# Kernel optimization log

Hardware: AMD Instinct MI355X
Metric: run time of the kernel (lower is better)

Reference implementation:

```python
import jax, jax.numpy as jnp
import numpy as np
import math

COND_DIM = 64
HIDDEN = 128
NUM_SIN = 2
SQRT2 = 1.4142135623730951


def fused_leaky_relu(x, bias):
    # stylegan2 fused bias + leaky relu (slope 0.2) with sqrt(2) gain
    return jax.nn.leaky_relu(x + bias, negative_slope=0.2) * SQRT2


def equal_linear2(x, W, b, lr_mul=1.0, activation=False):
    scale = lr_mul / math.sqrt(W.shape[1])
    out = x @ (W * scale).T
    if activation:
        return fused_leaky_relu(out, b * lr_mul)
    return out + b * lr_mul


def coords_to_sinusoidals(x, num_sinusoidals=NUM_SIN, multiplier=2.0):
    # x: [P, 1] -> [P, 2*num_sinusoidals], freq_type='mult': freqs = multiplier**i
    freqs = multiplier ** jnp.arange(num_sinusoidals, dtype=x.dtype)  # [S]
    ang = x * freqs  # [P, S]
    return jnp.concatenate([jnp.sin(ang), jnp.cos(ang)], axis=-1)


def setup_inputs() -> dict:
    key = jax.random.key(0)
    ks = jax.random.split(key, 10)
    B, N = 64, 8192
    coord_in = 2 * NUM_SIN  # 4
    in1 = coord_in + COND_DIM  # 68
    in2 = HIDDEN + COND_DIM    # 192
    coords = jax.random.normal(ks[0], (B, N, 2), dtype=jnp.float32)
    c = jax.random.normal(ks[1], (B, N, COND_DIM), dtype=jnp.float32)
    # EqualLinear2 weights init uniform(-1,1)/lr_mul; last layer zero in torch,
    # use small random values here so gradients/outputs are non-trivial.
    Wx1 = jax.random.uniform(ks[2], (HIDDEN, in1), minval=-1.0, maxval=1.0)
    bx1 = jnp.zeros((HIDDEN,), jnp.float32)
    Wx2 = jax.random.uniform(ks[3], (2, in2), minval=-1.0, maxval=1.0) * 0.1
    bx2 = jnp.zeros((2,), jnp.float32)
    Wy1 = jax.random.uniform(ks[4], (HIDDEN, in1), minval=-1.0, maxval=1.0)
    by1 = jnp.zeros((HIDDEN,), jnp.float32)
    Wy2 = jax.random.uniform(ks[5], (2, in2), minval=-1.0, maxval=1.0) * 0.1
    by2 = jnp.zeros((2,), jnp.float32)
    return {"coords": coords, "c": c,
            "Wx1": Wx1, "bx1": bx1, "Wx2": Wx2, "bx2": bx2,
            "Wy1": Wy1, "by1": by1, "Wy2": Wy2, "by2": by2}


def reference(coords, c, Wx1, bx1, Wx2, bx2, Wy1, by1, Wy2, by2):
    initial_shape = coords.shape[:-1]
    coords2 = coords.reshape(-1, coords.shape[-1])  # [P, 2]
    cf = c.reshape(-1, c.shape[-1])                 # [P, cond]
    x = coords2[:, 0:1]
    y = coords2[:, 1:2]

    # x branch -> affine params for y
    h = coords_to_sinusoidals(x / 10.0)
    h = equal_linear2(jnp.concatenate([h, cf], -1), Wx1, bx1, activation=True)
    o = equal_linear2(jnp.concatenate([h, cf], -1), Wx2, bx2, activation=False)
    y_log_scale = jnp.clip(o[:, 0:1], -5.0, 5.0)
    y_bias = o[:, 1:2]
    y = y * jnp.exp(y_log_scale) + y_bias

    # y branch -> affine params for x
    h = coords_to_sinusoidals(y / 10.0)
    h = equal_linear2(jnp.concatenate([h, cf], -1), Wy1, by1, activation=True)
    o = equal_linear2(jnp.concatenate([h, cf], -1), Wy2, by2, activation=False)
    x_log_scale = jnp.clip(o[:, 0:1], -5.0, 5.0)
    x_bias = o[:, 1:2]
    x = x * jnp.exp(x_log_scale) + x_bias

    warped = jnp.concatenate([x, y], -1).reshape(*initial_shape, -1)
    log_jac = jnp.concatenate([x_log_scale + y_log_scale], -1)
    log_jac = (x_log_scale + y_log_scale).reshape(*initial_shape, -1)
    return warped, log_jac
```

## Files before the change

### kernel.cpp

```cpp
#include <hip/hip_runtime.h>

typedef unsigned short u16t;
typedef short short8 __attribute__((ext_vector_type(8)));
typedef float f32x4 __attribute__((ext_vector_type(4)));

__device__ __forceinline__ u16t f2bf_rne(float f) {
  unsigned u = __builtin_bit_cast(unsigned, f);
  u += 0x7FFFu + ((u >> 16) & 1u);
  return (u16t)(u >> 16);
}
__device__ __forceinline__ unsigned pk2(float a, float b) {
  unsigned ua = __builtin_bit_cast(unsigned, a) + 0x8000u;
  unsigned ub = __builtin_bit_cast(unsigned, b) + 0x8000u;
  return (ua >> 16) | (ub & 0xFFFF0000u);
}
union S8U { short8 s; unsigned w[4]; };
__device__ __forceinline__ short8 pack8f(float4 a, float4 b) {
  S8U u;
  u.w[0] = pk2(a.x, a.y); u.w[1] = pk2(a.z, a.w);
  u.w[2] = pk2(b.x, b.y); u.w[3] = pk2(b.z, b.w);
  return u.s;
}

#define WS_WB  0
#define WS_BS  32768
#define WS_FF  49152
#define WS_BC  65536

__global__ void prep_kernel(const float* __restrict__ Wx1, const float* __restrict__ bx1,
                            const float* __restrict__ Wx2,
                            const float* __restrict__ Wy1, const float* __restrict__ by1,
                            const float* __restrict__ Wy2,
                            char* __restrict__ ws)
{
  const int tid = threadIdx.x;
  const int p = tid >> 9, nt = (tid >> 6) & 7, lane = tid & 63;
  const int l15 = lane & 15, quad = lane >> 4;
  const float* W1 = p ? Wy1 : Wx1;
  const float* B1 = p ? by1 : bx1;
  const float* W2 = p ? Wy2 : Wx2;
  const int n = nt * 16 + l15;
  const float* rp = W1 + n * 68;
  short8 bb0, bb1, bs = (short8)0;
  #pragma unroll
  for (int j = 0; j < 8; ++j) {
    bb0[j] = (short)f2bf_rne(rp[4 + quad * 8 + j]);
    bb1[j] = (short)f2bf_rne(rp[36 + quad * 8 + j]);
  }
  if (quad == 0) {
    #pragma unroll
    for (int j = 0; j < 4; ++j) bs[j] = (short)f2bf_rne(rp[j]);
  }
  short8* wb = (short8*)(ws + WS_WB);
  wb[((p * 8 + nt) * 2 + 0) * 64 + lane] = bb0;
  wb[((p * 8 + nt) * 2 + 1) * 64 + lane] = bb1;
  ((short8*)(ws + WS_BS))[(p * 8 + nt) * 64 + lane] = bs;
  const float SQ2 = 1.41421356237309515f;
  float4 ff;
  ff.x = B1[n]; ff.y = W2[n] * SQ2; ff.z = W2[192 + n] * SQ2; ff.w = 0.f;
  ((float4*)(ws + WS_FF))[(p * 8 + nt) * 64 + lane] = ff;

  if (tid < 256) {
    const int p2 = tid >> 7, h = (tid >> 6) & 1, ln = tid & 63;
    const int l2 = ln & 15, q2 = ln >> 4;
    const float* W2b = p2 ? Wy2 : Wx2;
    short8 bc = (short8)0;
    if (l2 < 2) {
      #pragma unroll
      for (int j = 0; j < 8; ++j)
        bc[j] = (short)f2bf_rne(W2b[l2 * 192 + 128 + h * 32 + q2 * 8 + j]);
    }
    ((short8*)(ws + WS_BC))[(p2 * 2 + h) * 64 + ln] = bc;
  }
}

__global__ __launch_bounds__(256, 4)
void icb_main(const float* __restrict__ g_coords, const float* __restrict__ g_c,
              const float* __restrict__ g_bx2, const float* __restrict__ g_by2,
              const char* __restrict__ ws, float* __restrict__ g_out)
{
  const int tid  = threadIdx.x;
  const int lane = tid & 63, wave = tid >> 6;
  const int l15  = lane & 15, quad = lane >> 4;
  const int wbase = blockIdx.x * 128 + wave * 32;

  const short8* wb  = (const short8*)(ws + WS_WB);
  const short8* wbs = (const short8*)(ws + WS_BS);
  const float4* wf  = (const float4*)(ws + WS_FF);
  const short8* wbc = (const short8*)(ws + WS_BC);

  short8 aC0[2], aC1[2];
  float xold[2], yold[2];
  #pragma unroll
  for (int mt = 0; mt < 2; ++mt) {
    const int r = wbase + mt * 16 + l15;
    const float4* cr = (const float4*)(g_c + (size_t)r * 64);
    float4 a0 = cr[quad * 2],     a1 = cr[quad * 2 + 1];
    float4 a2 = cr[8 + quad * 2], a3 = cr[8 + quad * 2 + 1];
    aC0[mt] = pack8f(a0, a1);
    aC1[mt] = pack8f(a2, a3);
    float2 p = ((const float2*)g_coords)[r];
    xold[mt] = p.x; yold[mt] = p.y;
  }

  const float s1 = 0.121267812518166f;
  const float s2 = 0.0721687836487032f;

  float vin[2], xnew[2], ynew[2], xls[2], yls[2];
  vin[0] = xold[0]; vin[1] = xold[1];

  #pragma unroll 1
  for (int path = 0; path < 2; ++path) {
    const int pb = path * 8;
    const float* b2 = path ? g_by2 : g_bx2;
    const float b20 = b2[0], b21 = b2[1];

    short8 aS[2];
    #pragma unroll
    for (int mt = 0; mt < 2; ++mt) {
      short8 f = (short8)0;
      if (quad == 0) {
        float a = vin[mt] * 0.1f;
        float sa, ca;
        __sincosf(a, &sa, &ca);
        float s2a = 2.0f * sa * ca;
        float c2a = 1.0f - 2.0f * sa * sa;
        f[0] = (short)f2bf_rne(sa); f[1] = (short)f2bf_rne(s2a);
        f[2] = (short)f2bf_rne(ca); f[3] = (short)f2bf_rne(c2a);
      }
      aS[mt] = f;
    }

    short8 bc0 = wbc[(path * 2 + 0) * 64 + lane];
    short8 bc1 = wbc[(path * 2 + 1) * 64 + lane];
    f32x4 acc8[2];
    #pragma unroll
    for (int mt = 0; mt < 2; ++mt) {
      f32x4 a = {0.f, 0.f, 0.f, 0.f};
      a = __builtin_amdgcn_mfma_f32_16x16x32_bf16(aC0[mt], bc0, a, 0, 0, 0);
      a = __builtin_amdgcn_mfma_f32_16x16x32_bf16(aC1[mt], bc1, a, 0, 0, 0);
      acc8[mt] = a;
    }

    float hp[2][4][2];
    #pragma unroll
    for (int mt = 0; mt < 2; ++mt)
      #pragma unroll
      for (int j = 0; j < 4; ++j) { hp[mt][j][0] = 0.f; hp[mt][j][1] = 0.f; }

    #pragma unroll 2
    for (int nt = 0; nt < 8; ++nt) {
      short8 bb0 = wb[((pb + nt) * 2 + 0) * 64 + lane];
      short8 bb1 = wb[((pb + nt) * 2 + 1) * 64 + lane];
      short8 bs  = wbs[(pb + nt) * 64 + lane];
      float4 ff  = wf[(pb + nt) * 64 + lane];
      #pragma unroll
      for (int mt = 0; mt < 2; ++mt) {
        f32x4 acc = {0.f, 0.f, 0.f, 0.f};
        acc = __builtin_amdgcn_mfma_f32_16x16x32_bf16(aC0[mt], bb0, acc, 0, 0, 0);
        acc = __builtin_amdgcn_mfma_f32_16x16x32_bf16(aC1[mt], bb1, acc, 0, 0, 0);
        acc = __builtin_amdgcn_mfma_f32_16x16x32_bf16(aS[mt],  bs,  acc, 0, 0, 0);
        #pragma unroll
        for (int j = 0; j < 4; ++j) {
          float v = fmaf(s1, acc[j], ff.x);
          float h = fmaxf(v, 0.2f * v);
          hp[mt][j][0] = fmaf(h, ff.y, hp[mt][j][0]);
          hp[mt][j][1] = fmaf(h, ff.z, hp[mt][j][1]);
        }
      }
    }

    #pragma unroll
    for (int mt = 0; mt < 2; ++mt)
      #pragma unroll
      for (int j = 0; j < 4; ++j) {
        hp[mt][j][0] += (l15 == 0) ? acc8[mt][j] : 0.f;
        hp[mt][j][1] += (l15 == 1) ? acc8[mt][j] : 0.f;
      }

    #pragma unroll
    for (int mt = 0; mt < 2; ++mt)
      #pragma unroll
      for (int j = 0; j < 4; ++j)
        #pragma unroll
        for (int o = 0; o < 2; ++o) {
          float v = hp[mt][j][o];
          v += __shfl_xor(v, 1);
          v += __shfl_xor(v, 2);
          v += __shfl_xor(v, 4);
          v += __shfl_xor(v, 8);
          hp[mt][j][o] = v;
        }

    const int jm = l15 & 3;
    const int src = ((l15 >> 2) << 4) | jm;
    #pragma unroll
    for (int mt = 0; mt < 2; ++mt) {
      float t0[4], t1[4];
      #pragma unroll
      for (int j = 0; j < 4; ++j) {
        t0[j] = fmaf(s2, hp[mt][j][0], b20);
        t1[j] = fmaf(s2, hp[mt][j][1], b21);
      }
      float s0 = (jm & 1) ? t0[1] : t0[0], s0b = (jm & 1) ? t0[3] : t0[2];
      s0 = (jm & 2) ? s0b : s0;
      float s1v = (jm & 1) ? t1[1] : t1[0], s1b = (jm & 1) ? t1[3] : t1[2];
      s1v = (jm & 2) ? s1b : s1v;
      float lsraw = __shfl(s0, src);
      float brow  = __shfl(s1v, src);

      float ls = fminf(fmaxf(lsraw, -5.f), 5.f);
      float e  = __expf(ls);
      if (path == 0) {
        yls[mt]  = ls;
        ynew[mt] = fmaf(yold[mt], e, brow);
        vin[mt]  = ynew[mt];
      } else {
        xls[mt]  = ls;
        xnew[mt] = fmaf(xold[mt], e, brow);
      }
    }
  }

  if (lane < 16) {
    #pragma unroll
    for (int mt = 0; mt < 2; ++mt) {
      int R = wbase + mt * 16 + lane;
      float2 pw; pw.x = xnew[mt]; pw.y = ynew[mt];
      reinterpret_cast<float2*>(g_out)[R] = pw;
      g_out[1048576 + R] = xls[mt] + yls[mt];
    }
  }
}

extern "C" void kernel_launch(void* const* d_in, const int* in_sizes, int n_in,
                              void* d_out, int out_size, void* d_ws, size_t ws_size,
                              hipStream_t stream) {
  (void)in_sizes; (void)n_in; (void)out_size; (void)ws_size;
  prep_kernel<<<1, 1024, 0, stream>>>(
      (const float*)d_in[2], (const float*)d_in[3], (const float*)d_in[4],
      (const float*)d_in[6], (const float*)d_in[7], (const float*)d_in[8],
      (char*)d_ws);
  icb_main<<<4096, 256, 0, stream>>>(
      (const float*)d_in[0], (const float*)d_in[1],
      (const float*)d_in[5], (const float*)d_in[9],
      (const char*)d_ws, (float*)d_out);
}
```

Before: 240.8 us.

## Double rows per wave, fold scales into weights, compact workspace, cheaper reductions

Each wave now handles 64 rows instead of 32, so every weight fragment loaded per nt step is reused across four M-tiles, and the grid is halved. The s1 and s2 scales are folded into the bf16 weights at prep time and bias1 seeds the MFMA accumulator, which removes per-element FMAs. The sin and bias-weight tables are stored compactly and loaded only by the lanes that need them. The output reduction packs both outputs into one shuffle tree, and launch bounds drop to 3 waves per SIMD to allow more registers. The trade-off is higher register pressure and lower occupancy.

Result: slower. 255.4 us (+6.1%).

```diff
diff --git a/kernel.cpp b/kernel.cpp
--- a/kernel.cpp
+++ b/kernel.cpp
@@ -22,10 +22,14 @@
   return u.s;
 }
 
-#define WS_WB  0
-#define WS_BS  32768
-#define WS_FF  49152
-#define WS_BC  65536
+#define WS_WB 0
+#define WS_BS 32768
+#define WS_FF 34816
+#define WS_BC 38912
+
+#define S1C   0.121267812518166f
+#define S2C   0.0721687836487032f
+#define SQ2S2 0.102062072615966f
 
 __global__ void prep_kernel(const float* __restrict__ Wx1, const float* __restrict__ bx1,
                             const float* __restrict__ Wx2,
@@ -41,40 +45,36 @@
   const float* W2 = p ? Wy2 : Wx2;
   const int n = nt * 16 + l15;
   const float* rp = W1 + n * 68;
-  short8 bb0, bb1, bs = (short8)0;
+  short8 bb0, bb1;
   #pragma unroll
   for (int j = 0; j < 8; ++j) {
-    bb0[j] = (short)f2bf_rne(rp[4 + quad * 8 + j]);
-    bb1[j] = (short)f2bf_rne(rp[36 + quad * 8 + j]);
-  }
-  if (quad == 0) {
-    #pragma unroll
-    for (int j = 0; j < 4; ++j) bs[j] = (short)f2bf_rne(rp[j]);
+    bb0[j] = (short)f2bf_rne(rp[4  + quad * 8 + j] * S1C);
+    bb1[j] = (short)f2bf_rne(rp[36 + quad * 8 + j] * S1C);
   }
   short8* wb = (short8*)(ws + WS_WB);
   wb[((p * 8 + nt) * 2 + 0) * 64 + lane] = bb0;
   wb[((p * 8 + nt) * 2 + 1) * 64 + lane] = bb1;
-  ((short8*)(ws + WS_BS))[(p * 8 + nt) * 64 + lane] = bs;
-  const float SQ2 = 1.41421356237309515f;
-  float4 ff;
-  ff.x = B1[n]; ff.y = W2[n] * SQ2; ff.z = W2[192 + n] * SQ2; ff.w = 0.f;
-  ((float4*)(ws + WS_FF))[(p * 8 + nt) * 64 + lane] = ff;
-
-  if (tid < 256) {
-    const int p2 = tid >> 7, h = (tid >> 6) & 1, ln = tid & 63;
-    const int l2 = ln & 15, q2 = ln >> 4;
+  if (quad == 0) {
+    ushort4 b4;
+    b4.x = f2bf_rne(rp[0] * S1C); b4.y = f2bf_rne(rp[1] * S1C);
+    b4.z = f2bf_rne(rp[2] * S1C); b4.w = f2bf_rne(rp[3] * S1C);
+    *(ushort4*)(ws + WS_BS + ((p * 8 + nt) * 16 + l15) * 8) = b4;
+    float4 ff;
+    ff.x = B1[n]; ff.y = W2[n] * SQ2S2; ff.z = W2[192 + n] * SQ2S2; ff.w = 0.f;
+    *(float4*)(ws + WS_FF + ((p * 8 + nt) * 16 + l15) * 16) = ff;
+  }
+  if (tid < 32) {
+    const int p2 = tid >> 4, h = (tid >> 3) & 1, l2 = (tid >> 2) & 1, q = tid & 3;
     const float* W2b = p2 ? Wy2 : Wx2;
-    short8 bc = (short8)0;
-    if (l2 < 2) {
-      #pragma unroll
-      for (int j = 0; j < 8; ++j)
-        bc[j] = (short)f2bf_rne(W2b[l2 * 192 + 128 + h * 32 + q2 * 8 + j]);
-    }
-    ((short8*)(ws + WS_BC))[(p2 * 2 + h) * 64 + ln] = bc;
-  }
-}
-
-__global__ __launch_bounds__(256, 4)
+    const float* src = W2b + l2 * 192 + 128 + h * 32 + q * 8;
+    short8 bc;
+    #pragma unroll
+    for (int j = 0; j < 8; ++j) bc[j] = (short)f2bf_rne(src[j] * S2C);
+    *(short8*)(ws + WS_BC + tid * 16) = bc;
+  }
+}
+
+__global__ __launch_bounds__(256, 3)
 void icb_main(const float* __restrict__ g_coords, const float* __restrict__ g_c,
               const float* __restrict__ g_bx2, const float* __restrict__ g_by2,
               const char* __restrict__ ws, float* __restrict__ g_out)
@@ -82,32 +82,25 @@
   const int tid  = threadIdx.x;
   const int lane = tid & 63, wave = tid >> 6;
   const int l15  = lane & 15, quad = lane >> 4;
-  const int wbase = blockIdx.x * 128 + wave * 32;
-
-  const short8* wb  = (const short8*)(ws + WS_WB);
-  const short8* wbs = (const short8*)(ws + WS_BS);
-  const float4* wf  = (const float4*)(ws + WS_FF);
-  const short8* wbc = (const short8*)(ws + WS_BC);
-
-  short8 aC0[2], aC1[2];
-  float xold[2], yold[2];
+  const int wbase = blockIdx.x * 256 + wave * 64;
+
+  const short8* wb = (const short8*)(ws + WS_WB);
+
+  short8 aC0[4], aC1[4];
+  float xold[4], yold[4];
   #pragma unroll
-  for (int mt = 0; mt < 2; ++mt) {
+  for (int mt = 0; mt < 4; ++mt) {
     const int r = wbase + mt * 16 + l15;
     const float4* cr = (const float4*)(g_c + (size_t)r * 64);
-    float4 a0 = cr[quad * 2],     a1 = cr[quad * 2 + 1];
-    float4 a2 = cr[8 + quad * 2], a3 = cr[8 + quad * 2 + 1];
-    aC0[mt] = pack8f(a0, a1);
-    aC1[mt] = pack8f(a2, a3);
-    float2 p = ((const float2*)g_coords)[r];
-    xold[mt] = p.x; yold[mt] = p.y;
-  }
-
-  const float s1 = 0.121267812518166f;
-  const float s2 = 0.0721687836487032f;
-
-  float vin[2], xnew[2], ynew[2], xls[2], yls[2];
-  vin[0] = xold[0]; vin[1] = xold[1];
+    aC0[mt] = pack8f(cr[quad * 2],     cr[quad * 2 + 1]);
+    aC1[mt] = pack8f(cr[8 + quad * 2], cr[8 + quad * 2 + 1]);
+    float2 pxy = ((const float2*)g_coords)[r];
+    xold[mt] = pxy.x; yold[mt] = pxy.y;
+  }
+
+  float vin[4], xnew[4], ynew[4], xls[4], yls[4];
+  #pragma unroll
+  for (int mt = 0; mt < 4; ++mt) vin[mt] = xold[mt];
 
   #pragma unroll 1
   for (int path = 0; path < 2; ++path) {
@@ -115,36 +108,30 @@
     const float* b2 = path ? g_by2 : g_bx2;
     const float b20 = b2[0], b21 = b2[1];
 
-    short8 aS[2];
-    #pragma unroll
-    for (int mt = 0; mt < 2; ++mt) {
+    short8 bc0 = (short8)0, bc1 = (short8)0;
+    if (l15 < 2) {
+      bc0 = *(const short8*)(ws + WS_BC + (path * 16 +     l15 * 4 + quad) * 16);
+      bc1 = *(const short8*)(ws + WS_BC + (path * 16 + 8 + l15 * 4 + quad) * 16);
+    }
+
+    short8 aS[4];
+    #pragma unroll
+    for (int mt = 0; mt < 4; ++mt) {
       short8 f = (short8)0;
       if (quad == 0) {
-        float a = vin[mt] * 0.1f;
-        float sa, ca;
-        __sincosf(a, &sa, &ca);
+        float a  = vin[mt] * 0.1f;
+        float sa = __sinf(a), ca = __cosf(a);
         float s2a = 2.0f * sa * ca;
-        float c2a = 1.0f - 2.0f * sa * sa;
+        float c2a = fmaf(-2.0f * sa, sa, 1.0f);
         f[0] = (short)f2bf_rne(sa); f[1] = (short)f2bf_rne(s2a);
         f[2] = (short)f2bf_rne(ca); f[3] = (short)f2bf_rne(c2a);
       }
       aS[mt] = f;
     }
 
-    short8 bc0 = wbc[(path * 2 + 0) * 64 + lane];
-    short8 bc1 = wbc[(path * 2 + 1) * 64 + lane];
-    f32x4 acc8[2];
-    #pragma unroll
-    for (int mt = 0; mt < 2; ++mt) {
-      f32x4 a = {0.f, 0.f, 0.f, 0.f};
-      a = __builtin_amdgcn_mfma_f32_16x16x32_bf16(aC0[mt], bc0, a, 0, 0, 0);
-      a = __builtin_amdgcn_mfma_f32_16x16x32_bf16(aC1[mt], bc1, a, 0, 0, 0);
-      acc8[mt] = a;
-    }
-
-    float hp[2][4][2];
-    #pragma unroll
-    for (int mt = 0; mt < 2; ++mt)
+    float hp[4][4][2];
+    #pragma unroll
+    for (int mt = 0; mt < 4; ++mt)
       #pragma unroll
       for (int j = 0; j < 4; ++j) { hp[mt][j][0] = 0.f; hp[mt][j][1] = 0.f; }
 
@@ -152,17 +139,22 @@
     for (int nt = 0; nt < 8; ++nt) {
       short8 bb0 = wb[((pb + nt) * 2 + 0) * 64 + lane];
       short8 bb1 = wb[((pb + nt) * 2 + 1) * 64 + lane];
-      short8 bs  = wbs[(pb + nt) * 64 + lane];
-      float4 ff  = wf[(pb + nt) * 64 + lane];
-      #pragma unroll
-      for (int mt = 0; mt < 2; ++mt) {
-        f32x4 acc = {0.f, 0.f, 0.f, 0.f};
+      short8 bs = (short8)0;
+      if (quad == 0) {
+        uint2 rw = *(const uint2*)(ws + WS_BS + ((pb + nt) * 16 + l15) * 8);
+        S8U u; u.w[0] = rw.x; u.w[1] = rw.y; u.w[2] = 0; u.w[3] = 0;
+        bs = u.s;
+      }
+      float4 ff = *(const float4*)(ws + WS_FF + ((pb + nt) * 16 + l15) * 16);
+      #pragma unroll
+      for (int mt = 0; mt < 4; ++mt) {
+        f32x4 acc = {ff.x, ff.x, ff.x, ff.x};
         acc = __builtin_amdgcn_mfma_f32_16x16x32_bf16(aC0[mt], bb0, acc, 0, 0, 0);
         acc = __builtin_amdgcn_mfma_f32_16x16x32_bf16(aC1[mt], bb1, acc, 0, 0, 0);
         acc = __builtin_amdgcn_mfma_f32_16x16x32_bf16(aS[mt],  bs,  acc, 0, 0, 0);
         #pragma unroll
         for (int j = 0; j < 4; ++j) {
-          float v = fmaf(s1, acc[j], ff.x);
+          float v = acc[j];
           float h = fmaxf(v, 0.2f * v);
           hp[mt][j][0] = fmaf(h, ff.y, hp[mt][j][0]);
           hp[mt][j][1] = fmaf(h, ff.z, hp[mt][j][1]);
@@ -170,44 +162,40 @@
       }
     }
 
-    #pragma unroll
-    for (int mt = 0; mt < 2; ++mt)
+    const float cinit = (l15 == 0) ? b20 : ((l15 == 1) ? b21 : 0.f);
+    #pragma unroll
+    for (int mt = 0; mt < 4; ++mt) {
+      f32x4 a = {cinit, cinit, cinit, cinit};
+      a = __builtin_amdgcn_mfma_f32_16x16x32_bf16(aC0[mt], bc0, a, 0, 0, 0);
+      a = __builtin_amdgcn_mfma_f32_16x16x32_bf16(aC1[mt], bc1, a, 0, 0, 0);
       #pragma unroll
       for (int j = 0; j < 4; ++j) {
-        hp[mt][j][0] += (l15 == 0) ? acc8[mt][j] : 0.f;
-        hp[mt][j][1] += (l15 == 1) ? acc8[mt][j] : 0.f;
-      }
-
-    #pragma unroll
-    for (int mt = 0; mt < 2; ++mt)
-      #pragma unroll
-      for (int j = 0; j < 4; ++j)
-        #pragma unroll
-        for (int o = 0; o < 2; ++o) {
-          float v = hp[mt][j][o];
-          v += __shfl_xor(v, 1);
-          v += __shfl_xor(v, 2);
-          v += __shfl_xor(v, 4);
-          v += __shfl_xor(v, 8);
-          hp[mt][j][o] = v;
-        }
-
-    const int jm = l15 & 3;
-    const int src = ((l15 >> 2) << 4) | jm;
-    #pragma unroll
-    for (int mt = 0; mt < 2; ++mt) {
-      float t0[4], t1[4];
+        hp[mt][j][0] += (l15 == 0) ? a[j] : 0.f;
+        hp[mt][j][1] += (l15 == 1) ? a[j] : 0.f;
+      }
+    }
+
+    const int jm   = l15 & 3;
+    const int srcA = ((l15 >> 2) << 4) | jm;
+    const int srcB = srcA | 8;
+    #pragma unroll
+    for (int mt = 0; mt < 4; ++mt) {
+      float mm[4];
       #pragma unroll
       for (int j = 0; j < 4; ++j) {
-        t0[j] = fmaf(s2, hp[mt][j][0], b20);
-        t1[j] = fmaf(s2, hp[mt][j][1], b21);
-      }
-      float s0 = (jm & 1) ? t0[1] : t0[0], s0b = (jm & 1) ? t0[3] : t0[2];
-      s0 = (jm & 2) ? s0b : s0;
-      float s1v = (jm & 1) ? t1[1] : t1[0], s1b = (jm & 1) ? t1[3] : t1[2];
-      s1v = (jm & 2) ? s1b : s1v;
-      float lsraw = __shfl(s0, src);
-      float brow  = __shfl(s1v, src);
+        float a = hp[mt][j][0], b = hp[mt][j][1];
+        a += __shfl_xor(a, 8);
+        b += __shfl_xor(b, 8);
+        float m = (l15 & 8) ? b : a;
+        m += __shfl_xor(m, 1);
+        m += __shfl_xor(m, 2);
+        m += __shfl_xor(m, 4);
+        mm[j] = m;
+      }
+      float msel = (jm & 2) ? ((jm & 1) ? mm[3] : mm[2])
+                            : ((jm & 1) ? mm[1] : mm[0]);
+      float lsraw = __shfl(msel, srcA);
+      float brow  = __shfl(msel, srcB);
 
       float ls = fminf(fmaxf(lsraw, -5.f), 5.f);
       float e  = __expf(ls);
@@ -224,7 +212,7 @@
 
   if (lane < 16) {
     #pragma unroll
-    for (int mt = 0; mt < 2; ++mt) {
+    for (int mt = 0; mt < 4; ++mt) {
       int R = wbase + mt * 16 + lane;
       float2 pw; pw.x = xnew[mt]; pw.y = ynew[mt];
       reinterpret_cast<float2*>(g_out)[R] = pw;
@@ -241,7 +229,7 @@
       (const float*)d_in[2], (const float*)d_in[3], (const float*)d_in[4],
       (const float*)d_in[6], (const float*)d_in[7], (const float*)d_in[8],
       (char*)d_ws);
-  icb_main<<<4096, 256, 0, stream>>>(
+  icb_main<<<2048, 256, 0, stream>>>(
       (const float*)d_in[0], (const float*)d_in[1],
       (const float*)d_in[5], (const float*)d_in[9],
       (const char*)d_ws, (float*)d_out);
```
